# Kernel optimization log

Measured on AMD Instinct MI355X. Metric: run time of the kernel, lower is better.

Reference implementation:

```python
import jax, jax.numpy as jnp
import numpy as np

B, C, H, W = 4, 128, 56, 56
K = 7
K2 = K * K
RATIO = 16


def _conv1x1(x, w, b=None):
    # x: [B,C,H,W], w: [O,C]
    y = jnp.einsum('oc,bchw->bohw', w, x)
    return y if b is None else y + b[None, :, None, None]


def _dwconv(x, w, dil, pad):
    # depthwise conv, w: [C,1,k,k]
    return jax.lax.conv_general_dilated(
        x, w, window_strides=(1, 1), padding=[(pad, pad), (pad, pad)],
        rhs_dilation=(dil, dil), feature_group_count=x.shape[1],
        dimension_numbers=('NCHW', 'OIHW', 'NCHW'))


def _bn(x, s, b):
    # inference-mode BatchNorm folded to per-channel affine
    return x * s[None, :, None, None] + b[None, :, None, None]


def setup_inputs() -> dict:
    key = jax.random.key(0)
    ks = jax.random.split(key, 16)
    w = 0.05  # weight scale
    inp = {
        'x_up': jax.random.normal(ks[0], (B, C, H, W), jnp.float32),
        'x_skip': jax.random.normal(ks[1], (B, C, H, W), jnp.float32),
        'wq': jax.random.normal(ks[2], (C, C), jnp.float32) * w,
        'bq': jnp.zeros((C,), jnp.float32),
        'wk': jax.random.normal(ks[3], (C, C), jnp.float32) * w,
        'bk': jnp.zeros((C,), jnp.float32),
        'wv': jax.random.normal(ks[4], (C, C), jnp.float32) * w,
        'bv': jnp.zeros((C,), jnp.float32),
        'ww': jax.random.normal(ks[5], (K2, 49), jnp.float32) * w,
        'bw': jnp.zeros((K2,), jnp.float32),
        'lk_w': jax.random.normal(ks[6], (C, 1, K, K), jnp.float32) * 0.1,
        'lk_bn_s': jax.random.uniform(ks[7], (C,), jnp.float32, 0.5, 1.5),
        'lk_bn_b': jnp.zeros((C,), jnp.float32),
        'dw5': jax.random.normal(ks[8], (C, 1, 5, 5), jnp.float32) * 0.1,
        'bn5_s': jax.random.uniform(ks[7], (C,), jnp.float32, 0.5, 1.5),
        'bn5_b': jnp.zeros((C,), jnp.float32),
        'dw3a': jax.random.normal(ks[9], (C, 1, 3, 3), jnp.float32) * 0.1,
        'bn3a_s': jax.random.uniform(ks[9], (C,), jnp.float32, 0.5, 1.5),
        'bn3a_b': jnp.zeros((C,), jnp.float32),
        'dw3b': jax.random.normal(ks[10], (C, 1, 3, 3), jnp.float32) * 0.1,
        'bn3b_s': jax.random.uniform(ks[10], (C,), jnp.float32, 0.5, 1.5),
        'bn3b_b': jnp.zeros((C,), jnp.float32),
        'dw3c': jax.random.normal(ks[11], (C, 1, 3, 3), jnp.float32) * 0.1,
        'bn3c_s': jax.random.uniform(ks[11], (C,), jnp.float32, 0.5, 1.5),
        'bn3c_b': jnp.zeros((C,), jnp.float32),
        'lepe_bn_s': jax.random.uniform(ks[12], (C,), jnp.float32, 0.5, 1.5),
        'lepe_bn_b': jnp.zeros((C,), jnp.float32),
        'gate_w': jax.random.normal(ks[13], (C, C), jnp.float32) * w,
        'gate_bn_s': jax.random.uniform(ks[13], (C,), jnp.float32, 0.5, 1.5),
        'gate_bn_b': jnp.zeros((C,), jnp.float32),
        'fus_w': jax.random.normal(ks[14], (C, C), jnp.float32) * w,
        'fus_b': jnp.zeros((C,), jnp.float32),
        'ca_w1': jax.random.normal(ks[15], (C // RATIO, C), jnp.float32) * w,
        'ca_w2': jax.random.normal(ks[15], (C, C // RATIO), jnp.float32) * w,
        'res_scale': jnp.ones((1,), jnp.float32),
    }
    return inp


def _forward(x_up, x_skip, wq, bq, wk, bk, wv, bv, ww, bw,
             lk_w, lk_bn_s, lk_bn_b, dw5, bn5_s, bn5_b,
             dw3a, bn3a_s, bn3a_b, dw3b, bn3b_s, bn3b_b, dw3c, bn3c_s, bn3c_b,
             lepe_bn_s, lepe_bn_b, gate_w, gate_bn_s, gate_bn_b,
             fus_w, fus_b, ca_w1, ca_w2, res_scale):
    identity = x_skip

    # ---- lepe: DilatedReparamBlock (lk 7x7 dw + 4 dilated dw branches, each BN) + final BN
    out = _bn(_dwconv(x_skip, lk_w, 1, 3), lk_bn_s, lk_bn_b)
    out = out + _bn(_dwconv(x_skip, dw5, 1, 2), bn5_s, bn5_b)    # k=5, d=1
    out = out + _bn(_dwconv(x_skip, dw3a, 1, 1), bn3a_s, bn3a_b)  # k=3, d=1
    out = out + _bn(_dwconv(x_skip, dw3b, 2, 2), bn3b_s, bn3b_b)  # k=3, d=2
    out = out + _bn(_dwconv(x_skip, dw3c, 3, 3), bn3c_s, bn3c_b)  # k=3, d=3
    lepe = _bn(out, lepe_bn_s, lepe_bn_b)

    # ---- gate: 1x1 conv (no bias) -> BN -> SiLU
    gate = jax.nn.silu(_bn(_conv1x1(x_skip, gate_w), gate_bn_s, gate_bn_b))

    # ---- q / k / v
    query = _conv1x1(x_skip, wq, bq)                              # [B,C,H,W]
    # AdaptiveAvgPool2d(7): H,W divisible by 7 -> block mean
    pooled = x_up.reshape(B, C, 7, H // 7, 7, W // 7).mean(axis=(3, 5))  # [B,C,7,7]
    key_t = _conv1x1(pooled, wk, bk).reshape(B, C, 49)            # [B,C,49]
    value = _conv1x1(x_skip, wv, bv)                              # [B,C,H,W]

    # ---- attention over 49 pooled key tokens
    scale = float(C) ** -0.5
    q_r = query.reshape(B, C, H * W).transpose(0, 2, 1)           # [B,HW,C]
    attn = jax.nn.softmax(jnp.einsum('bnc,bcl->bnl', q_r, key_t) * scale, axis=-1)
    attn_r = attn.transpose(0, 2, 1).reshape(B, 49, H, W)         # [B,49,H,W]
    dyn_w = jnp.einsum('ol,blhw->bohw', ww, attn_r) + bw[None, :, None, None]  # [B,K2,H,W]

    # ---- unfold value (k=7, pad=3), torch layout: channel-major, (kh,kw) row-major
    pad = K // 2
    vp = jnp.pad(value, ((0, 0), (0, 0), (pad, pad), (pad, pad)))
    patches = jnp.stack([vp[:, :, i:i + H, j:j + W]
                         for i in range(K) for j in range(K)], axis=2)  # [B,C,K2,H,W]
    mixed = jnp.einsum('bkhw,bckhw->bchw', dyn_w, patches)

    x_fused = _conv1x1(mixed, fus_w, fus_b) + lepe

    # ---- channel attention (shared MLP on avg & max pooled)
    avg = x_fused.mean(axis=(2, 3))                               # [B,C]
    mx = x_fused.max(axis=(2, 3))                                 # [B,C]
    def ca_mlp(v):
        return jnp.einsum('cr,br->bc', ca_w2, jax.nn.relu(jnp.einsum('rc,bc->br', ca_w1, v)))
    ca = jax.nn.sigmoid(ca_mlp(avg) + ca_mlp(mx))[:, :, None, None]
    x_fused = ca * x_fused

    return gate * x_fused + identity * res_scale


def reference(x_up, x_skip, wq, bq, wk, bk, wv, bv, ww, bw,
              lk_w, lk_bn_s, lk_bn_b, dw5, bn5_s, bn5_b,
              dw3a, bn3a_s, bn3a_b, dw3b, bn3b_s, bn3b_b, dw3c, bn3c_s, bn3c_b,
              lepe_bn_s, lepe_bn_b, gate_w, gate_bn_s, gate_bn_b,
              fus_w, fus_b, ca_w1, ca_w2, res_scale):
    return _forward(x_up, x_skip, wq, bq, wk, bk, wv, bv, ww, bw,
                    lk_w, lk_bn_s, lk_bn_b, dw5, bn5_s, bn5_b,
                    dw3a, bn3a_s, bn3a_b, dw3b, bn3b_s, bn3b_b, dw3c, bn3c_s, bn3c_b,
                    lepe_bn_s, lepe_bn_b, gate_w, gate_bn_s, gate_bn_b,
                    fus_w, fus_b, ca_w1, ca_w2, res_scale)
```

## Files before the change

### kernel.cpp

```cpp
#include <hip/hip_runtime.h>

typedef unsigned int u32;

#define HW 3136
#define SCALE 0.08838834764831843f

#define OFF_W7    0
#define OFF_BIAS  6272
#define OFF_POOL  6400
#define OFF_MT    31488
#define OFF_D     56576
#define OFF_AVG   56772
#define OFF_MAXU  57284
#define OFF_CA    57796
#define OFF_WC    58308
#define OFF_BC    74692
#define OFF_FV    74820
#define OFF_GATE  1680452
#define OFF_DYN   3286084
#define OFF_XF    3900740

struct Params {
  const float *x_up, *x_skip, *wq, *bq, *wk, *bk, *wv, *bv, *ww, *bw;
  const float *lk_w, *lk_s, *lk_b, *dw5, *s5, *b5, *dw3a, *s3a, *b3a,
              *dw3b, *s3b, *b3b, *dw3c, *s3c, *b3c, *lepe_s, *lepe_b;
  const float *gate_w, *gate_s, *gate_b, *fus_w, *fus_b, *ca_w1, *ca_w2, *res;
  float* W;
  float* out;
};

__device__ __forceinline__ u32 fenc(float f){
  union{float f; u32 u;} v; v.f = f;
  return (v.u & 0x80000000u) ? ~v.u : (v.u | 0x80000000u);
}
__device__ __forceinline__ float fdec(u32 u){
  union{float f; u32 uu;} v;
  v.uu = (u & 0x80000000u) ? (u ^ 0x80000000u) : ~u;
  return v.f;
}

__global__ __launch_bounds__(256) void k_prep(Params P){
  float* W = P.W;
  const int tid = threadIdx.x, blk = blockIdx.x;
  if (blk < 128){
    const int b = blk >> 5, c0 = (blk & 31) * 4;
    if (tid < 196){
      const int ci = tid / 49, l = tid % 49;
      const int c = c0 + ci, i = l / 7, j = l % 7;
      const float* src = P.x_up + (size_t)(b*128 + c)*HW + (i*8)*56 + j*8;
      float s = 0.f;
      #pragma unroll
      for (int di=0; di<8; ++di){
        const float4 a0 = *(const float4*)(src + di*56);
        const float4 a1 = *(const float4*)(src + di*56 + 4);
        s += a0.x+a0.y+a0.z+a0.w + a1.x+a1.y+a1.z+a1.w;
      }
      W[OFF_POOL + (size_t)(b*128+c)*49 + l] = s * (1.f/64.f);
    }
  } else if (blk == 128){
    for (int idx = tid; idx < 6272; idx += 256){
      const int c = idx/49, k = idx%49;
      const int dy = k/7 - 3, dx = k%7 - 3;
      float w = P.lk_s[c] * P.lk_w[c*49 + k];
      if (dy>=-2 && dy<=2 && dx>=-2 && dx<=2)
        w += P.s5[c] * P.dw5[c*25 + (dy+2)*5 + (dx+2)];
      if (dy>=-1 && dy<=1 && dx>=-1 && dx<=1)
        w += P.s3a[c] * P.dw3a[c*9 + (dy+1)*3 + (dx+1)];
      if ((dy==-2||dy==0||dy==2) && (dx==-2||dx==0||dx==2))
        w += P.s3b[c] * P.dw3b[c*9 + (dy/2+1)*3 + (dx/2+1)];
      if ((dy==-3||dy==0||dy==3) && (dx==-3||dx==0||dx==3))
        w += P.s3c[c] * P.dw3c[c*9 + (dy/3+1)*3 + (dx/3+1)];
      W[OFF_W7 + idx] = P.lepe_s[c] * w;
    }
    if (tid < 128){
      const float bs = P.lk_b[tid] + P.b5[tid] + P.b3a[tid] + P.b3b[tid] + P.b3c[tid];
      W[OFF_BIAS + tid] = P.lepe_s[tid] * bs + P.lepe_b[tid] + P.fus_b[tid];
    }
    for (int i = tid; i < 512; i += 256){
      W[OFF_AVG + i] = 0.f;
      ((u32*)W + OFF_MAXU)[i] = fenc(-1e30f);
    }
  } else if (blk < 193){
    const int o = (blk - 129)*2 + (tid >> 7), c = tid & 127;
    float a = 0.f;
    #pragma unroll 8
    for (int m=0;m<128;++m) a += P.fus_w[o*128+m] * P.wv[m*128+c];
    W[OFF_WC + o*128 + c] = a;
  } else {
    if (tid < 128){
      float a = 0.f;
      #pragma unroll 8
      for (int m=0;m<128;++m) a += P.fus_w[tid*128+m] * P.bv[m];
      W[OFF_BC + tid] = a;
    }
  }
}

__global__ __launch_bounds__(128) void k_key(Params P){
  __shared__ float pc[128], kc[128], red[128];
  float* W = P.W;
  const int b = blockIdx.x / 49, l = blockIdx.x % 49;
  const int t = threadIdx.x;
  pc[t] = W[OFF_POOL + (size_t)(b*128+t)*49 + l];
  __syncthreads();
  float acc = P.bk[t];
  const float4* wr = (const float4*)(P.wk + t*128);
  #pragma unroll 8
  for (int k0=0;k0<32;++k0){
    const float4 w = wr[k0];
    acc += w.x*pc[k0*4] + w.y*pc[k0*4+1] + w.z*pc[k0*4+2] + w.w*pc[k0*4+3];
  }
  kc[t] = acc;
  red[t] = P.bq[t] * acc;
  __syncthreads();
  float m = 0.f;
  #pragma unroll 8
  for (int c=0;c<128;++c) m += P.wq[c*128 + t] * kc[c];
  W[OFF_MT + (size_t)b*6272 + t*49 + l] = m * SCALE;
  if (t < 64) red[t] += red[t+64];
  __syncthreads();
  if (t < 32) red[t] += red[t+32];
  __syncthreads();
  if (t < 16) red[t] += red[t+16];
  __syncthreads();
  if (t < 8) red[t] += red[t+8];
  __syncthreads();
  if (t < 4) red[t] += red[t+4];
  __syncthreads();
  if (t == 0) W[OFF_D + b*49 + l] = (red[0]+red[1]+red[2]+red[3]) * SCALE;
}

__global__ __launch_bounds__(256, 4) void k_gemm(Params P){
  __shared__ float xl[128][36];
  __shared__ float wl[32][132];
  float* W = P.W;
  const int tid = threadIdx.x;
  const int x = blockIdx.x, xcd = x & 7;
  const int b = xcd >> 1;
  const int p0 = ((xcd & 1) + 2*(x >> 3)) * 32;
  const int mat = blockIdx.y;
  const float* __restrict__ wsrc = mat ? P.gate_w : (W + OFF_WC);

  for (int idx = tid; idx < 1024; idx += 256){
    const int c = idx >> 3, pq = idx & 7;
    *(float4*)&xl[c][pq*4] =
        *(const float4*)(P.x_skip + (size_t)(b*128+c)*HW + p0 + pq*4);
  }

  const int oq = tid >> 2, pq = tid & 3;
  const int o0 = oq*2, px = pq*8;
  float i0 = 0.f, i1 = 0.f;
  if (mat == 0){ i0 = W[OFF_BC + o0]; i1 = W[OFF_BC + o0 + 1]; }
  float a0[8], a1[8];
  #pragma unroll
  for (int j=0;j<8;++j){ a0[j]=i0; a1[j]=i1; }

  for (int g=0; g<4; ++g){
    __syncthreads();
    for (int idx = tid; idx < 1024; idx += 256){
      const int o = idx >> 3, kq = idx & 7;
      const float4 v = *(const float4*)(wsrc + (size_t)o*128 + g*32 + kq*4);
      wl[kq*4+0][o] = v.x; wl[kq*4+1][o] = v.y;
      wl[kq*4+2][o] = v.z; wl[kq*4+3][o] = v.w;
    }
    __syncthreads();
    #pragma unroll 8
    for (int k=0;k<32;++k){
      const float2 w2 = *(const float2*)&wl[k][o0];
      const float4 xa = *(const float4*)&xl[g*32+k][px];
      const float4 xb = *(const float4*)&xl[g*32+k][px+4];
      const float xv[8] = {xa.x,xa.y,xa.z,xa.w, xb.x,xb.y,xb.z,xb.w};
      #pragma unroll
      for (int j=0;j<8;++j){ a0[j] += w2.x*xv[j]; a1[j] += w2.y*xv[j]; }
    }
  }
  if (mat == 0){
    float* d0 = W + OFF_FV + (size_t)(b*128 + o0)*HW + p0 + px;
    float* d1 = W + OFF_FV + (size_t)(b*128 + o0 + 1)*HW + p0 + px;
    float4 v;
    v.x=a0[0];v.y=a0[1];v.z=a0[2];v.w=a0[3]; *(float4*)d0 = v;
    v.x=a0[4];v.y=a0[5];v.z=a0[6];v.w=a0[7]; *(float4*)(d0+4) = v;
    v.x=a1[0];v.y=a1[1];v.z=a1[2];v.w=a1[3]; *(float4*)d1 = v;
    v.x=a1[4];v.y=a1[5];v.z=a1[6];v.w=a1[7]; *(float4*)(d1+4) = v;
  } else {
    const float s0 = P.gate_s[o0], s1 = P.gate_s[o0+1];
    const float c0 = P.gate_b[o0], c1 = P.gate_b[o0+1];
    #pragma unroll
    for (int j=0;j<8;++j){
      float y0 = s0*a0[j] + c0, y1 = s1*a1[j] + c1;
      a0[j] = y0 / (1.f + __expf(-y0));
      a1[j] = y1 / (1.f + __expf(-y1));
    }
    float* d0 = W + OFF_GATE + (size_t)(b*128 + o0)*HW + p0 + px;
    float* d1 = W + OFF_GATE + (size_t)(b*128 + o0 + 1)*HW + p0 + px;
    float4 v;
    v.x=a0[0];v.y=a0[1];v.z=a0[2];v.w=a0[3]; *(float4*)d0 = v;
    v.x=a0[4];v.y=a0[5];v.z=a0[6];v.w=a0[7]; *(float4*)(d0+4) = v;
    v.x=a1[0];v.y=a1[1];v.z=a1[2];v.w=a1[3]; *(float4*)d1 = v;
    v.x=a1[4];v.y=a1[5];v.z=a1[6];v.w=a1[7]; *(float4*)(d1+4) = v;
  }
}

__global__ __launch_bounds__(256, 3) void k_attn(Params P){
  __shared__ float xl[128][16];
  __shared__ float mtl[128][52];
  __shared__ float wwl[49][52];
  __shared__ float attl[16][52];
  __shared__ float dvl[52];
  float* W = P.W;
  const int tid = threadIdx.x;
  const int x = blockIdx.x, xcd = x & 7;
  const int b = xcd >> 1;
  const int p0 = ((xcd & 1) + 2*(x >> 3)) * 16;

  for (int idx = tid; idx < 512; idx += 256){
    const int c = idx >> 2, pq = idx & 3;
    *(float4*)&xl[c][pq*4] =
        *(const float4*)(P.x_skip + (size_t)(b*128+c)*HW + p0 + pq*4);
  }
  for (int idx = tid; idx < 6272; idx += 256)
    mtl[idx/49][idx%49] = W[OFF_MT + (size_t)b*6272 + idx];
  for (int idx = tid; idx < 2401; idx += 256)
    wwl[idx/49][idx%49] = P.ww[idx];
  if (tid < 49) dvl[tid] = W[OFF_D + b*49 + tid];
  __syncthreads();

  const int px = tid >> 4, sub = tid & 15;
  const int l0 = sub, l1 = sub+16, l2 = sub+32, l3 = sub+48;
  const int l3c = (l3 < 49) ? l3 : 51;
  float lv0 = dvl[l0], lv1 = dvl[l1], lv2 = dvl[l2];
  float lv3 = (l3 < 49) ? dvl[l3] : -1e30f;
  float a3 = 0.f;
  #pragma unroll 4
  for (int c=0;c<128;++c){
    const float xv = xl[c][px];
    lv0 += mtl[c][l0]*xv;
    lv1 += mtl[c][l1]*xv;
    lv2 += mtl[c][l2]*xv;
    a3  += mtl[c][l3c]*xv;
  }
  if (l3 < 49) lv3 += a3;

  float m = fmaxf(fmaxf(lv0, lv1), fmaxf(lv2, lv3));
  #pragma unroll
  for (int d=1; d<16; d<<=1) m = fmaxf(m, __shfl_xor(m, d, 64));
  const float e0 = __expf(lv0-m), e1 = __expf(lv1-m), e2 = __expf(lv2-m);
  const float e3 = (l3 < 49) ? __expf(lv3-m) : 0.f;
  float s = e0+e1+e2+e3;
  #pragma unroll
  for (int d=1; d<16; d<<=1) s += __shfl_xor(s, d, 64);
  const float inv = 1.f / s;
  attl[px][l0] = e0*inv;
  attl[px][l1] = e1*inv;
  attl[px][l2] = e2*inv;
  if (l3 < 49) attl[px][l3] = e3*inv;
  __syncthreads();

  #pragma unroll
  for (int j=0;j<4;++j){
    const int oo = sub + 16*j;
    if (oo < 49){
      float a = P.bw[oo];
      #pragma unroll 7
      for (int l=0;l<49;++l) a += wwl[oo][l] * attl[px][l];
      W[OFF_DYN + (size_t)(b*49+oo)*HW + p0 + px] = a;
    }
  }
}

__global__ __launch_bounds__(256, 2) void k_mix(Params P){
  __shared__ float fvt[8][14][64];
  __shared__ float xst[8][14][64];
  __shared__ float w7l[8][49];
  __shared__ float b2l[8];
  float* W = P.W;
  const int tid = threadIdx.x;
  const int x = blockIdx.x, xcd = x & 7;
  const int b = xcd >> 1;
  const int u = (xcd & 1) + 2*(x >> 3);
  const int band = u % 7, chg = u / 7;
  const int c0 = chg*8, r0 = band*8;

  const int row = tid / 28, cp = tid % 28;
  const int col0 = cp*2;
  const int pxg = (r0 + row)*56 + col0;
  const bool act = tid < 224;

  float2 dr[49];
  if (act){
    #pragma unroll
    for (int k=0;k<49;++k)
      dr[k] = *(const float2*)(W + OFF_DYN + (size_t)(b*49+k)*HW + pxg);
  }

  for (int idx = tid; idx < 1792; idx += 256){
    const int cc = idx / 224, rem = idx % 224;
    const int rr = rem >> 4, cq = rem & 15;
    const int gr = r0 - 3 + rr, gcs = cq*4 - 4;
    float4 vf = {0.f,0.f,0.f,0.f}, vx = {0.f,0.f,0.f,0.f};
    if ((unsigned)gr < 56u){
      const size_t basef = OFF_FV + (size_t)(b*128 + c0 + cc)*HW + gr*56;
      const size_t basex = (size_t)(b*128 + c0 + cc)*HW + gr*56;
      if (gcs >= 0 && gcs + 3 < 56){
        vf = *(const float4*)(W + basef + gcs);
        vx = *(const float4*)(P.x_skip + basex + gcs);
      } else {
        float tf[4], tx[4];
        #pragma unroll
        for (int e=0;e<4;++e){
          const int gc = gcs + e;
          const bool v = (unsigned)gc < 56u;
          tf[e] = v ? W[basef + gc] : 0.f;
          tx[e] = v ? P.x_skip[basex + gc] : 0.f;
        }
        vf.x=tf[0];vf.y=tf[1];vf.z=tf[2];vf.w=tf[3];
        vx.x=tx[0];vx.y=tx[1];vx.z=tx[2];vx.w=tx[3];
      }
    }
    *(float4*)&fvt[cc][rr][cq*4] = vf;
    *(float4*)&xst[cc][rr][cq*4] = vx;
  }
  for (int idx = tid; idx < 392; idx += 256)
    w7l[idx/49][idx%49] = W[OFF_W7 + (c0 + idx/49)*49 + idx%49];
  if (tid < 8) b2l[tid] = W[OFF_BIAS + c0 + tid];
  __syncthreads();

  float a0[8], a1[8];
  if (act){
    #pragma unroll
    for (int c=0;c<8;++c){ a0[c] = b2l[c]; a1[c] = b2l[c]; }
    #pragma unroll
    for (int c=0;c<8;++c){
      #pragma unroll
      for (int i=0;i<7;++i){
        const float2 f0 = *(const float2*)&fvt[c][row+i][col0];
        const float2 f1 = *(const float2*)&fvt[c][row+i][col0+2];
        const float2 f2 = *(const float2*)&fvt[c][row+i][col0+4];
        const float2 f3 = *(const float2*)&fvt[c][row+i][col0+6];
        const float2 f4 = *(const float2*)&fvt[c][row+i][col0+8];
        const float2 g0 = *(const float2*)&xst[c][row+i][col0];
        const float2 g1 = *(const float2*)&xst[c][row+i][col0+2];
        const float2 g2 = *(const float2*)&xst[c][row+i][col0+4];
        const float2 g3 = *(const float2*)&xst[c][row+i][col0+6];
        const float2 g4 = *(const float2*)&xst[c][row+i][col0+8];
        const float f[10] = {f0.x,f0.y,f1.x,f1.y,f2.x,f2.y,f3.x,f3.y,f4.x,f4.y};
        const float gg[10] = {g0.x,g0.y,g1.x,g1.y,g2.x,g2.y,g3.x,g3.y,g4.x,g4.y};
        #pragma unroll
        for (int j=0;j<7;++j){
          const float dx0 = dr[i*7+j].x, dx1 = dr[i*7+j].y;
          const float w7 = w7l[c][i*7+j];
          a0[c] += dx0 * f[1+j] + w7 * gg[1+j];
          a1[c] += dx1 * f[2+j] + w7 * gg[2+j];
        }
      }
    }
    #pragma unroll
    for (int c=0;c<8;++c){
      float2 v; v.x = a0[c]; v.y = a1[c];
      *(float2*)(W + OFF_XF + (size_t)(b*128 + c0 + c)*HW + pxg) = v;
    }
  }
  #pragma unroll
  for (int c=0;c<8;++c){
    float s = act ? (a0[c] + a1[c]) : 0.f;
    float mm = act ? fmaxf(a0[c], a1[c]) : -1e30f;
    #pragma unroll
    for (int d=1; d<64; d<<=1){
      s += __shfl_xor(s, d, 64);
      mm = fmaxf(mm, __shfl_xor(mm, d, 64));
    }
    if ((tid & 63) == 0){
      atomicAdd(W + OFF_AVG + b*128 + c0 + c, s);
      atomicMax((u32*)W + OFF_MAXU + b*128 + c0 + c, fenc(mm));
    }
  }
}

__global__ __launch_bounds__(512) void k_ca(Params P){
  __shared__ float avl[512], mxl[512], hl[64];
  float* W = P.W;
  const int tid = threadIdx.x;
  avl[tid] = W[OFF_AVG + tid] * (1.f/3136.f);
  mxl[tid] = fdec(((u32*)W + OFF_MAXU)[tid]);
  __syncthreads();
  if (tid < 64){
    const int b = tid >> 4, which = (tid >> 3) & 1, r = tid & 7;
    const float* v = (which ? mxl : avl) + b*128;
    float a = 0.f;
    const float4* wr = (const float4*)(P.ca_w1 + r*128);
    for (int k0=0;k0<32;++k0){
      const float4 w4 = wr[k0];
      a += w4.x*v[k0*4] + w4.y*v[k0*4+1] + w4.z*v[k0*4+2] + w4.w*v[k0*4+3];
    }
    hl[tid] = fmaxf(a, 0.f);
  }
  __syncthreads();
  {
    const int b = tid >> 7, c = tid & 127;
    float a = 0.f;
    #pragma unroll
    for (int r=0;r<8;++r) a += P.ca_w2[c*8+r] * (hl[b*16+r] + hl[b*16+8+r]);
    W[OFF_CA + tid] = 1.f/(1.f + __expf(-a));
  }
}

__global__ __launch_bounds__(256) void k_final(Params P){
  float* W = P.W;
  const int tid = threadIdx.x;
  const int b = blockIdx.y;
  const int ofs = blockIdx.x*1024 + tid*4;
  const int c = ofs / 3136;
  const size_t gi = (size_t)b*401408 + ofs;
  const float ca = W[OFF_CA + b*128 + c];
  const float res = P.res[0];
  const float4 gv = *(const float4*)(W + OFF_GATE + gi);
  const float4 xv = *(const float4*)(W + OFF_XF + gi);
  const float4 sk = *(const float4*)(P.x_skip + gi);
  float4 ov;
  ov.x = gv.x*xv.x*ca + sk.x*res;
  ov.y = gv.y*xv.y*ca + sk.y*res;
  ov.z = gv.z*xv.z*ca + sk.z*res;
  ov.w = gv.w*xv.w*ca + sk.w*res;
  *(float4*)(P.out + gi) = ov;
}

extern "C" void kernel_launch(void* const* d_in, const int* in_sizes, int n_in,
                              void* d_out, int out_size, void* d_ws, size_t ws_size,
                              hipStream_t stream){
  Params P;
  const float* const* in = (const float* const*)d_in;
  P.x_up = in[0];  P.x_skip = in[1]; P.wq = in[2];  P.bq = in[3];
  P.wk = in[4];    P.bk = in[5];     P.wv = in[6];  P.bv = in[7];
  P.ww = in[8];    P.bw = in[9];
  P.lk_w = in[10]; P.lk_s = in[11];  P.lk_b = in[12];
  P.dw5 = in[13];  P.s5 = in[14];    P.b5 = in[15];
  P.dw3a = in[16]; P.s3a = in[17];   P.b3a = in[18];
  P.dw3b = in[19]; P.s3b = in[20];   P.b3b = in[21];
  P.dw3c = in[22]; P.s3c = in[23];   P.b3c = in[24];
  P.lepe_s = in[25]; P.lepe_b = in[26];
  P.gate_w = in[27]; P.gate_s = in[28]; P.gate_b = in[29];
  P.fus_w = in[30];  P.fus_b = in[31];
  P.ca_w1 = in[32];  P.ca_w2 = in[33]; P.res = in[34];
  P.W = (float*)d_ws;
  P.out = (float*)d_out;

  hipLaunchKernelGGL(k_prep,  dim3(194),   dim3(256), 0, stream, P);
  hipLaunchKernelGGL(k_key,   dim3(196),   dim3(128), 0, stream, P);
  hipLaunchKernelGGL(k_gemm,  dim3(392,2), dim3(256), 0, stream, P);
  hipLaunchKernelGGL(k_attn,  dim3(784),   dim3(256), 0, stream, P);
  hipLaunchKernelGGL(k_mix,   dim3(448),   dim3(256), 0, stream, P);
  hipLaunchKernelGGL(k_ca,    dim3(1),     dim3(512), 0, stream, P);
  hipLaunchKernelGGL(k_final, dim3(392,4), dim3(256), 0, stream, P);
}
```

Measured before the change: 284.0 us.

## Increase grid parallelism across prep, gemm and mix kernels with finer tiles

k_prep now pools x_up with one block per (batch, channel), staging the full plane in shared memory and summing in four parts. k_gemm halves its pixel tile to 16 so twice as many blocks run. k_attn drops padded shared arrays in favour of dense float4 loads. k_mix is restructured to two channels per block over 14-row quarter tiles, reloading dynamic weights per row with float4 loads. The aim is to fill more CUs on the MI355X, at the cost of reloading weights and dynamic data more often and losing some register reuse.

```diff
diff --git a/kernel.cpp b/kernel.cpp
--- a/kernel.cpp
+++ b/kernel.cpp
@@ -40,24 +40,40 @@
 }
 
 __global__ __launch_bounds__(256) void k_prep(Params P){
+  __shared__ float pl[3136];
+  __shared__ float part[208];
   float* W = P.W;
   const int tid = threadIdx.x, blk = blockIdx.x;
-  if (blk < 128){
-    const int b = blk >> 5, c0 = (blk & 31) * 4;
+  if (blk < 512){
+    const int b = blk >> 7, c = blk & 127;
+    const float* src = P.x_up + (size_t)(b*128 + c)*HW;
+    for (int idx = tid; idx < 784; idx += 256)
+      *(float4*)&pl[idx*4] = *(const float4*)(src + idx*4);
+    __syncthreads();
     if (tid < 196){
-      const int ci = tid / 49, l = tid % 49;
-      const int c = c0 + ci, i = l / 7, j = l % 7;
-      const float* src = P.x_up + (size_t)(b*128 + c)*HW + (i*8)*56 + j*8;
-      float s = 0.f;
+      const int l = tid >> 2, s = tid & 3;
+      const int i = l/7, j = l%7;
+      float sm = 0.f;
       #pragma unroll
-      for (int di=0; di<8; ++di){
-        const float4 a0 = *(const float4*)(src + di*56);
-        const float4 a1 = *(const float4*)(src + di*56 + 4);
-        s += a0.x+a0.y+a0.z+a0.w + a1.x+a1.y+a1.z+a1.w;
+      for (int r=0;r<2;++r){
+        const int base = (8*i + 2*s + r)*56 + 8*j;
+        #pragma unroll
+        for (int e=0;e<8;++e) sm += pl[base+e];
       }
-      W[OFF_POOL + (size_t)(b*128+c)*49 + l] = s * (1.f/64.f);
-    }
-  } else if (blk == 128){
+      part[tid] = sm;
+    }
+    __syncthreads();
+    if (tid < 49){
+      const float sm = part[tid*4] + part[tid*4+1] + part[tid*4+2] + part[tid*4+3];
+      W[OFF_POOL + (size_t)(b*128+c)*49 + tid] = sm * (1.f/64.f);
+    }
+  } else if (blk < 576){
+    const int o = (blk - 512)*2 + (tid >> 7), c = tid & 127;
+    float a = 0.f;
+    #pragma unroll 8
+    for (int m=0;m<128;++m) a += P.fus_w[o*128+m] * P.wv[m*128+c];
+    W[OFF_WC + o*128 + c] = a;
+  } else if (blk == 576){
     for (int idx = tid; idx < 6272; idx += 256){
       const int c = idx/49, k = idx%49;
       const int dy = k/7 - 3, dx = k%7 - 3;
@@ -80,12 +96,6 @@
       W[OFF_AVG + i] = 0.f;
       ((u32*)W + OFF_MAXU)[i] = fenc(-1e30f);
     }
-  } else if (blk < 193){
-    const int o = (blk - 129)*2 + (tid >> 7), c = tid & 127;
-    float a = 0.f;
-    #pragma unroll 8
-    for (int m=0;m<128;++m) a += P.fus_w[o*128+m] * P.wv[m*128+c];
-    W[OFF_WC + o*128 + c] = a;
   } else {
     if (tid < 128){
       float a = 0.f;
@@ -130,30 +140,30 @@
   if (t == 0) W[OFF_D + b*49 + l] = (red[0]+red[1]+red[2]+red[3]) * SCALE;
 }
 
-__global__ __launch_bounds__(256, 4) void k_gemm(Params P){
-  __shared__ float xl[128][36];
-  __shared__ float wl[32][132];
+__global__ __launch_bounds__(256) void k_gemm(Params P){
+  __shared__ float xl[128][20];
+  __shared__ float wl[32][133];
   float* W = P.W;
   const int tid = threadIdx.x;
   const int x = blockIdx.x, xcd = x & 7;
   const int b = xcd >> 1;
-  const int p0 = ((xcd & 1) + 2*(x >> 3)) * 32;
+  const int p0 = ((xcd & 1) + 2*(x >> 3)) * 16;
   const int mat = blockIdx.y;
   const float* __restrict__ wsrc = mat ? P.gate_w : (W + OFF_WC);
 
-  for (int idx = tid; idx < 1024; idx += 256){
-    const int c = idx >> 3, pq = idx & 7;
+  for (int idx = tid; idx < 512; idx += 256){
+    const int c = idx >> 2, pq = idx & 3;
     *(float4*)&xl[c][pq*4] =
         *(const float4*)(P.x_skip + (size_t)(b*128+c)*HW + p0 + pq*4);
   }
 
   const int oq = tid >> 2, pq = tid & 3;
-  const int o0 = oq*2, px = pq*8;
+  const int o0 = oq*2, px = pq*4;
   float i0 = 0.f, i1 = 0.f;
   if (mat == 0){ i0 = W[OFF_BC + o0]; i1 = W[OFF_BC + o0 + 1]; }
-  float a0[8], a1[8];
+  float a0[4], a1[4];
   #pragma unroll
-  for (int j=0;j<8;++j){ a0[j]=i0; a1[j]=i1; }
+  for (int j=0;j<4;++j){ a0[j]=i0; a1[j]=i1; }
 
   for (int g=0; g<4; ++g){
     __syncthreads();
@@ -167,44 +177,37 @@
     #pragma unroll 8
     for (int k=0;k<32;++k){
       const float2 w2 = *(const float2*)&wl[k][o0];
-      const float4 xa = *(const float4*)&xl[g*32+k][px];
-      const float4 xb = *(const float4*)&xl[g*32+k][px+4];
-      const float xv[8] = {xa.x,xa.y,xa.z,xa.w, xb.x,xb.y,xb.z,xb.w};
+      const float4 x4 = *(const float4*)&xl[g*32+k][px];
+      const float xv[4] = {x4.x,x4.y,x4.z,x4.w};
       #pragma unroll
-      for (int j=0;j<8;++j){ a0[j] += w2.x*xv[j]; a1[j] += w2.y*xv[j]; }
+      for (int j=0;j<4;++j){ a0[j] += w2.x*xv[j]; a1[j] += w2.y*xv[j]; }
     }
   }
   if (mat == 0){
-    float* d0 = W + OFF_FV + (size_t)(b*128 + o0)*HW + p0 + px;
-    float* d1 = W + OFF_FV + (size_t)(b*128 + o0 + 1)*HW + p0 + px;
-    float4 v;
-    v.x=a0[0];v.y=a0[1];v.z=a0[2];v.w=a0[3]; *(float4*)d0 = v;
-    v.x=a0[4];v.y=a0[5];v.z=a0[6];v.w=a0[7]; *(float4*)(d0+4) = v;
-    v.x=a1[0];v.y=a1[1];v.z=a1[2];v.w=a1[3]; *(float4*)d1 = v;
-    v.x=a1[4];v.y=a1[5];v.z=a1[6];v.w=a1[7]; *(float4*)(d1+4) = v;
+    float4 v0 = {a0[0],a0[1],a0[2],a0[3]};
+    float4 v1 = {a1[0],a1[1],a1[2],a1[3]};
+    *(float4*)(W + OFF_FV + (size_t)(b*128+o0  )*HW + p0 + px) = v0;
+    *(float4*)(W + OFF_FV + (size_t)(b*128+o0+1)*HW + p0 + px) = v1;
   } else {
     const float s0 = P.gate_s[o0], s1 = P.gate_s[o0+1];
     const float c0 = P.gate_b[o0], c1 = P.gate_b[o0+1];
     #pragma unroll
-    for (int j=0;j<8;++j){
+    for (int j=0;j<4;++j){
       float y0 = s0*a0[j] + c0, y1 = s1*a1[j] + c1;
       a0[j] = y0 / (1.f + __expf(-y0));
       a1[j] = y1 / (1.f + __expf(-y1));
     }
-    float* d0 = W + OFF_GATE + (size_t)(b*128 + o0)*HW + p0 + px;
-    float* d1 = W + OFF_GATE + (size_t)(b*128 + o0 + 1)*HW + p0 + px;
-    float4 v;
-    v.x=a0[0];v.y=a0[1];v.z=a0[2];v.w=a0[3]; *(float4*)d0 = v;
-    v.x=a0[4];v.y=a0[5];v.z=a0[6];v.w=a0[7]; *(float4*)(d0+4) = v;
-    v.x=a1[0];v.y=a1[1];v.z=a1[2];v.w=a1[3]; *(float4*)d1 = v;
-    v.x=a1[4];v.y=a1[5];v.z=a1[6];v.w=a1[7]; *(float4*)(d1+4) = v;
-  }
-}
-
-__global__ __launch_bounds__(256, 3) void k_attn(Params P){
+    float4 v0 = {a0[0],a0[1],a0[2],a0[3]};
+    float4 v1 = {a1[0],a1[1],a1[2],a1[3]};
+    *(float4*)(W + OFF_GATE + (size_t)(b*128+o0  )*HW + p0 + px) = v0;
+    *(float4*)(W + OFF_GATE + (size_t)(b*128+o0+1)*HW + p0 + px) = v1;
+  }
+}
+
+__global__ __launch_bounds__(256) void k_attn(Params P){
   __shared__ float xl[128][16];
-  __shared__ float mtl[128][52];
-  __shared__ float wwl[49][52];
+  __shared__ float mtl[6272];
+  __shared__ float wwl[2401];
   __shared__ float attl[16][52];
   __shared__ float dvl[52];
   float* W = P.W;
@@ -218,26 +221,27 @@
     *(float4*)&xl[c][pq*4] =
         *(const float4*)(P.x_skip + (size_t)(b*128+c)*HW + p0 + pq*4);
   }
-  for (int idx = tid; idx < 6272; idx += 256)
-    mtl[idx/49][idx%49] = W[OFF_MT + (size_t)b*6272 + idx];
-  for (int idx = tid; idx < 2401; idx += 256)
-    wwl[idx/49][idx%49] = P.ww[idx];
+  for (int idx = tid; idx < 1568; idx += 256)
+    *(float4*)&mtl[idx*4] = *(const float4*)(W + OFF_MT + (size_t)b*6272 + idx*4);
+  for (int idx = tid; idx < 600; idx += 256)
+    *(float4*)&wwl[idx*4] = *(const float4*)(P.ww + idx*4);
+  if (tid == 0) wwl[2400] = P.ww[2400];
   if (tid < 49) dvl[tid] = W[OFF_D + b*49 + tid];
   __syncthreads();
 
   const int px = tid >> 4, sub = tid & 15;
   const int l0 = sub, l1 = sub+16, l2 = sub+32, l3 = sub+48;
-  const int l3c = (l3 < 49) ? l3 : 51;
+  const int l3c = (l3 < 49) ? l3 : 48;
   float lv0 = dvl[l0], lv1 = dvl[l1], lv2 = dvl[l2];
   float lv3 = (l3 < 49) ? dvl[l3] : -1e30f;
   float a3 = 0.f;
   #pragma unroll 4
   for (int c=0;c<128;++c){
     const float xv = xl[c][px];
-    lv0 += mtl[c][l0]*xv;
-    lv1 += mtl[c][l1]*xv;
-    lv2 += mtl[c][l2]*xv;
-    a3  += mtl[c][l3c]*xv;
+    lv0 += mtl[c*49+l0]*xv;
+    lv1 += mtl[c*49+l1]*xv;
+    lv2 += mtl[c*49+l2]*xv;
+    a3  += mtl[c*49+l3c]*xv;
   }
   if (l3 < 49) lv3 += a3;
 
@@ -262,116 +266,113 @@
     if (oo < 49){
       float a = P.bw[oo];
       #pragma unroll 7
-      for (int l=0;l<49;++l) a += wwl[oo][l] * attl[px][l];
+      for (int l=0;l<49;++l) a += wwl[oo*49+l] * attl[px][l];
       W[OFF_DYN + (size_t)(b*49+oo)*HW + p0 + px] = a;
     }
   }
 }
 
-__global__ __launch_bounds__(256, 2) void k_mix(Params P){
-  __shared__ float fvt[8][14][64];
-  __shared__ float xst[8][14][64];
-  __shared__ float w7l[8][49];
-  __shared__ float b2l[8];
+__global__ __launch_bounds__(256) void k_mix(Params P){
+  __shared__ float fvs[2][20][64];
+  __shared__ float xss[2][20][64];
+  __shared__ float w7s[2][49];
   float* W = P.W;
   const int tid = threadIdx.x;
-  const int x = blockIdx.x, xcd = x & 7;
+  const int blk = blockIdx.x, xcd = blk & 7;
   const int b = xcd >> 1;
-  const int u = (xcd & 1) + 2*(x >> 3);
-  const int band = u % 7, chg = u / 7;
-  const int c0 = chg*8, r0 = band*8;
-
-  const int row = tid / 28, cp = tid % 28;
-  const int col0 = cp*2;
-  const int pxg = (r0 + row)*56 + col0;
-  const bool act = tid < 224;
-
-  float2 dr[49];
-  if (act){
-    #pragma unroll
-    for (int k=0;k<49;++k)
-      dr[k] = *(const float2*)(W + OFF_DYN + (size_t)(b*49+k)*HW + pxg);
-  }
-
-  for (int idx = tid; idx < 1792; idx += 256){
-    const int cc = idx / 224, rem = idx % 224;
+  const int idx2 = blk >> 3;
+  const int cp = idx2 >> 1;
+  const int qt = (xcd & 1) + 2*(idx2 & 1);
+  const int c0 = cp*2, r0 = qt*14;
+
+  for (int idx = tid; idx < 1280; idx += 256){
+    const int a2 = idx / 320;
+    const int ch = a2 & 1, arr = a2 >> 1;
+    const int rem = idx % 320;
     const int rr = rem >> 4, cq = rem & 15;
-    const int gr = r0 - 3 + rr, gcs = cq*4 - 4;
-    float4 vf = {0.f,0.f,0.f,0.f}, vx = {0.f,0.f,0.f,0.f};
+    const int gr = r0 - 3 + rr, gc0 = cq*4 - 4;
+    float4 v = {0.f,0.f,0.f,0.f};
     if ((unsigned)gr < 56u){
-      const size_t basef = OFF_FV + (size_t)(b*128 + c0 + cc)*HW + gr*56;
-      const size_t basex = (size_t)(b*128 + c0 + cc)*HW + gr*56;
-      if (gcs >= 0 && gcs + 3 < 56){
-        vf = *(const float4*)(W + basef + gcs);
-        vx = *(const float4*)(P.x_skip + basex + gcs);
+      const float* src = arr ? (P.x_skip + (size_t)(b*128 + c0 + ch)*HW + gr*56)
+                             : (W + OFF_FV + (size_t)(b*128 + c0 + ch)*HW + gr*56);
+      if (gc0 >= 0 && gc0 + 3 < 56){
+        v = *(const float4*)(src + gc0);
       } else {
-        float tf[4], tx[4];
+        float t[4];
         #pragma unroll
         for (int e=0;e<4;++e){
-          const int gc = gcs + e;
-          const bool v = (unsigned)gc < 56u;
-          tf[e] = v ? W[basef + gc] : 0.f;
-          tx[e] = v ? P.x_skip[basex + gc] : 0.f;
+          const int gc = gc0 + e;
+          t[e] = ((unsigned)gc < 56u) ? src[gc] : 0.f;
         }
-        vf.x=tf[0];vf.y=tf[1];vf.z=tf[2];vf.w=tf[3];
-        vx.x=tx[0];vx.y=tx[1];vx.z=tx[2];vx.w=tx[3];
+        v.x=t[0]; v.y=t[1]; v.z=t[2]; v.w=t[3];
       }
     }
-    *(float4*)&fvt[cc][rr][cq*4] = vf;
-    *(float4*)&xst[cc][rr][cq*4] = vx;
-  }
-  for (int idx = tid; idx < 392; idx += 256)
-    w7l[idx/49][idx%49] = W[OFF_W7 + (c0 + idx/49)*49 + idx%49];
-  if (tid < 8) b2l[tid] = W[OFF_BIAS + c0 + tid];
-  __syncthreads();
-
-  float a0[8], a1[8];
+    if (arr) *(float4*)&xss[ch][rr][cq*4] = v;
+    else     *(float4*)&fvs[ch][rr][cq*4] = v;
+  }
+  if (tid < 98) w7s[tid/49][tid%49] = W[OFF_W7 + (c0 + tid/49)*49 + tid%49];
+  __syncthreads();
+
+  const bool act = tid < 196;
+  const int row = tid / 14, q = tid % 14;
+  const int q4 = q*4;
+  const int grow = r0 + row;
+  float acc[2][4];
+  {
+    const float b0 = W[OFF_BIAS + c0], b1 = W[OFF_BIAS + c0 + 1];
+    #pragma unroll
+    for (int e=0;e<4;++e){ acc[0][e] = b0; acc[1][e] = b1; }
+  }
   if (act){
-    #pragma unroll
-    for (int c=0;c<8;++c){ a0[c] = b2l[c]; a1[c] = b2l[c]; }
-    #pragma unroll
-    for (int c=0;c<8;++c){
+    const float* dynb = W + OFF_DYN + (size_t)b*49*HW + grow*56 + q4;
+    #pragma unroll
+    for (int i=0;i<7;++i){
+      float4 dr[7];
       #pragma unroll
-      for (int i=0;i<7;++i){
-        const float2 f0 = *(const float2*)&fvt[c][row+i][col0];
-        const float2 f1 = *(const float2*)&fvt[c][row+i][col0+2];
-        const float2 f2 = *(const float2*)&fvt[c][row+i][col0+4];
-        const float2 f3 = *(const float2*)&fvt[c][row+i][col0+6];
-        const float2 f4 = *(const float2*)&fvt[c][row+i][col0+8];
-        const float2 g0 = *(const float2*)&xst[c][row+i][col0];
-        const float2 g1 = *(const float2*)&xst[c][row+i][col0+2];
-        const float2 g2 = *(const float2*)&xst[c][row+i][col0+4];
-        const float2 g3 = *(const float2*)&xst[c][row+i][col0+6];
-        const float2 g4 = *(const float2*)&xst[c][row+i][col0+8];
-        const float f[10] = {f0.x,f0.y,f1.x,f1.y,f2.x,f2.y,f3.x,f3.y,f4.x,f4.y};
-        const float gg[10] = {g0.x,g0.y,g1.x,g1.y,g2.x,g2.y,g3.x,g3.y,g4.x,g4.y};
+      for (int j=0;j<7;++j)
+        dr[j] = *(const float4*)(dynb + (size_t)(i*7+j)*HW);
+      #pragma unroll
+      for (int ch=0;ch<2;++ch){
+        float fw[12], xw[12];
+        {
+          float4 t;
+          t = *(const float4*)&fvs[ch][row+i][q4];    fw[0]=t.x;fw[1]=t.y;fw[2]=t.z;fw[3]=t.w;
+          t = *(const float4*)&fvs[ch][row+i][q4+4];  fw[4]=t.x;fw[5]=t.y;fw[6]=t.z;fw[7]=t.w;
+          t = *(const float4*)&fvs[ch][row+i][q4+8];  fw[8]=t.x;fw[9]=t.y;fw[10]=t.z;fw[11]=t.w;
+          t = *(const float4*)&xss[ch][row+i][q4];    xw[0]=t.x;xw[1]=t.y;xw[2]=t.z;xw[3]=t.w;
+          t = *(const float4*)&xss[ch][row+i][q4+4];  xw[4]=t.x;xw[5]=t.y;xw[6]=t.z;xw[7]=t.w;
+          t = *(const float4*)&xss[ch][row+i][q4+8];  xw[8]=t.x;xw[9]=t.y;xw[10]=t.z;xw[11]=t.w;
+        }
         #pragma unroll
         for (int j=0;j<7;++j){
-          const float dx0 = dr[i*7+j].x, dx1 = dr[i*7+j].y;
-          const float w7 = w7l[c][i*7+j];
-          a0[c] += dx0 * f[1+j] + w7 * gg[1+j];
-          a1[c] += dx1 * f[2+j] + w7 * gg[2+j];
+          const float4 dv = dr[j];
+          const float wv = w7s[ch][i*7+j];
+          acc[ch][0] += dv.x*fw[j+1] + wv*xw[j+1];
+          acc[ch][1] += dv.y*fw[j+2] + wv*xw[j+2];
+          acc[ch][2] += dv.z*fw[j+3] + wv*xw[j+3];
+          acc[ch][3] += dv.w*fw[j+4] + wv*xw[j+4];
         }
       }
     }
     #pragma unroll
-    for (int c=0;c<8;++c){
-      float2 v; v.x = a0[c]; v.y = a1[c];
-      *(float2*)(W + OFF_XF + (size_t)(b*128 + c0 + c)*HW + pxg) = v;
+    for (int ch=0;ch<2;++ch){
+      float4 v = {acc[ch][0], acc[ch][1], acc[ch][2], acc[ch][3]};
+      *(float4*)(W + OFF_XF + (size_t)(b*128 + c0 + ch)*HW + grow*56 + q4) = v;
     }
   }
   #pragma unroll
-  for (int c=0;c<8;++c){
-    float s = act ? (a0[c] + a1[c]) : 0.f;
-    float mm = act ? fmaxf(a0[c], a1[c]) : -1e30f;
+  for (int ch=0;ch<2;++ch){
+    float s = act ? (acc[ch][0]+acc[ch][1]+acc[ch][2]+acc[ch][3]) : 0.f;
+    float mm = act ? fmaxf(fmaxf(acc[ch][0],acc[ch][1]),
+                           fmaxf(acc[ch][2],acc[ch][3])) : -1e30f;
     #pragma unroll
     for (int d=1; d<64; d<<=1){
       s += __shfl_xor(s, d, 64);
       mm = fmaxf(mm, __shfl_xor(mm, d, 64));
     }
     if ((tid & 63) == 0){
-      atomicAdd(W + OFF_AVG + b*128 + c0 + c, s);
-      atomicMax((u32*)W + OFF_MAXU + b*128 + c0 + c, fenc(mm));
+      atomicAdd(W + OFF_AVG + b*128 + c0 + ch, s);
+      atomicMax((u32*)W + OFF_MAXU + b*128 + c0 + ch, fenc(mm));
     }
   }
 }
@@ -444,11 +445,11 @@
   P.W = (float*)d_ws;
   P.out = (float*)d_out;
 
-  hipLaunchKernelGGL(k_prep,  dim3(194),   dim3(256), 0, stream, P);
+  hipLaunchKernelGGL(k_prep,  dim3(578),   dim3(256), 0, stream, P);
   hipLaunchKernelGGL(k_key,   dim3(196),   dim3(128), 0, stream, P);
-  hipLaunchKernelGGL(k_gemm,  dim3(392,2), dim3(256), 0, stream, P);
+  hipLaunchKernelGGL(k_gemm,  dim3(784,2), dim3(256), 0, stream, P);
   hipLaunchKernelGGL(k_attn,  dim3(784),   dim3(256), 0, stream, P);
-  hipLaunchKernelGGL(k_mix,   dim3(448),   dim3(256), 0, stream, P);
+  hipLaunchKernelGGL(k_mix,   dim3(1024),  dim3(256), 0, stream, P);
   hipLaunchKernelGGL(k_ca,    dim3(1),     dim3(512), 0, stream, P);
   hipLaunchKernelGGL(k_final, dim3(392,4), dim3(256), 0, stream, P);
 }
```

New measurement: 268.8 us. -5.4%, faster.
